# Kernel tuning notes

Hardware: AMD Instinct MI355X
Metric: run time of the kernel (lower is better)

## Reference

```python
import jax, jax.numpy as jnp
import numpy as np

V, E, HID, T = 50000, 512, 1024, 16   # vocab, embed_dim, hidden_dim, tagset
H = HID // 2                          # per-direction LSTM hidden
B, S = 32, 512                        # batch, seq_len
NEG = -10000.0                        # start/stop transitions are set to -10000 in __init__


def setup_inputs() -> dict:
    key = jax.random.key(0)
    ks = jax.random.split(key, 12)
    g = lambda i, shape, scale: (jax.random.normal(ks[i], shape, jnp.float32) * scale)
    return {
        "sentence": jax.random.randint(ks[0], (B, S), 0, V),
        "embedding": g(1, (V, E), 1.0),
        # PyTorch LSTM gate order i,f,g,o; bias fused (b_ih + b_hh)
        "Wih_f": g(2, (4 * H, E), 0.04), "Whh_f": g(3, (4 * H, H), 0.04), "b_f": g(4, (4 * H,), 0.04),
        "Wih_b": g(5, (4 * H, E), 0.04), "Whh_b": g(6, (4 * H, H), 0.04), "b_b": g(7, (4 * H,), 0.04),
        "W_out": g(8, (T, HID), 0.04), "b_out": g(9, (T,), 0.04),
        "transitions": g(10, (T, T), 0.35),   # xavier_normal-ish
        "start_trans": jnp.full((T,), NEG, jnp.float32),
        "stop_trans": jnp.full((T,), NEG, jnp.float32),
    }


def _lstm_dir(x, Wih, Whh, b, reverse):
    # x: [B, S, E] -> h sequence [B, S, H]
    bsz, hid = x.shape[0], Whh.shape[1]

    def step(carry, xt):
        h, c = carry
        gates = xt @ Wih.T + h @ Whh.T + b          # [B, 4H]
        i, f, gg, o = jnp.split(gates, 4, axis=-1)
        c = jax.nn.sigmoid(f) * c + jax.nn.sigmoid(i) * jnp.tanh(gg)
        h = jax.nn.sigmoid(o) * jnp.tanh(c)
        return (h, c), h

    init = (jnp.zeros((bsz, hid), x.dtype), jnp.zeros((bsz, hid), x.dtype))
    _, hs = jax.lax.scan(step, init, jnp.swapaxes(x, 0, 1), reverse=reverse)
    return jnp.swapaxes(hs, 0, 1)


def _features(sentence, embedding, Wih_f, Whh_f, b_f, Wih_b, Whh_b, b_b, W_out, b_out):
    emb = embedding[sentence]                                  # [B, S, E]
    hf = _lstm_dir(emb, Wih_f, Whh_f, b_f, reverse=False)      # [B, S, H]
    hb = _lstm_dir(emb, Wih_b, Whh_b, b_b, reverse=True)       # [B, S, H]
    return jnp.concatenate([hf, hb], -1) @ W_out.T + b_out     # [B, S, T]


def reference(sentence, embedding, Wih_f, Whh_f, b_f, Wih_b, Whh_b, b_b,
              W_out, b_out, transitions, start_trans, stop_trans):
    feats = _features(sentence, embedding, Wih_f, Whh_f, b_f,
                      Wih_b, Whh_b, b_b, W_out, b_out)         # [B, S, T]

    # ---- Viterbi DP (forward pass with backpointers) ----
    v0 = feats[:, 0] + start_trans                             # [B, T]

    def step(v, feat):
        scores = v[:, :, None] + transitions[None]             # [B, Tprev, Tcur]
        idx = jnp.argmax(scores, axis=1)                       # [B, T] backpointers
        v = jnp.max(scores, axis=1) + feat
        return v, idx

    v, idxs = jax.lax.scan(step, v0, jnp.swapaxes(feats[:, 1:], 0, 1))  # idxs: [S-1, B, T]
    last = jnp.argmax(v + stop_trans, axis=-1)                 # [B]

    # ---- backtrace ----
    def back(tag, idx):
        prev = jnp.take_along_axis(idx, tag[:, None], axis=1)[:, 0]
        return prev, prev

    _, prevs = jax.lax.scan(back, last, idxs, reverse=True)    # [S-1, B]
    tags = jnp.concatenate([jnp.swapaxes(prevs, 0, 1), last[:, None]], axis=1)  # [B, S]
    return tags
```

## Files before the change

kernel.cpp:

```cpp
#include <hip/hip_runtime.h>
#include <stdint.h>

#define BATCH 32
#define SEQ   512
#define EDIM  512
#define HID   512
#define NG    2048
#define NTAG  16

typedef _Float16 f16;
typedef _Float16 f16x4 __attribute__((ext_vector_type(4)));
typedef _Float16 f16x8 __attribute__((ext_vector_type(8)));
typedef float    f32x4 __attribute__((ext_vector_type(4)));

#define LO_SCALE 2048.0f
#define LO_INV   (1.0f/2048.0f)

__global__ __launch_bounds__(256) void k_split4(
    const float* __restrict__ s0, const float* __restrict__ s1,
    const float* __restrict__ s2, const float* __restrict__ s3,
    f16* __restrict__ wih_hi, f16* __restrict__ wih_lo,
    f16* __restrict__ whh_hi, f16* __restrict__ whh_lo) {
    const int y = blockIdx.y;
    const float* src = (y == 0) ? s0 : (y == 1) ? s1 : (y == 2) ? s2 : s3;
    f16* hi = ((y < 2) ? wih_hi : whh_hi) + (size_t)(y & 1) * NG * EDIM;
    f16* lo = ((y < 2) ? wih_lo : whh_lo) + (size_t)(y & 1) * NG * EDIM;
    int i = blockIdx.x * blockDim.x + threadIdx.x;
    int stride = gridDim.x * blockDim.x;
    for (; i < NG*EDIM; i += stride) {
        float x = src[i];
        f16 h = (f16)x;
        hi[i] = h;
        lo[i] = (f16)((x - (float)h) * LO_SCALE);
    }
}

__global__ __launch_bounds__(256) void k_gather(const int* __restrict__ sent,
                                                const float* __restrict__ emb,
                                                f16* __restrict__ ehi, f16* __restrict__ elo) {
    int m = blockIdx.x;
    int idx = sent[m];
    const float* src = emb + (size_t)idx * EDIM;
    int k = threadIdx.x * 2;
    float2 v = *(const float2*)(src + k);
    f16 h0 = (f16)v.x, h1 = (f16)v.y;
    ehi[(size_t)m*EDIM + k]     = h0;
    ehi[(size_t)m*EDIM + k + 1] = h1;
    elo[(size_t)m*EDIM + k]     = (f16)((v.x - (float)h0) * LO_SCALE);
    elo[(size_t)m*EDIM + k + 1] = (f16)((v.y - (float)h1) * LO_SCALE);
}

__device__ __forceinline__ void gld16(const void* g, void* l) {
    __builtin_amdgcn_global_load_lds((const __attribute__((address_space(1))) uint32_t*)g,
                                     (__attribute__((address_space(3))) uint32_t*)l, 16, 0, 0);
}
__device__ __forceinline__ f32x4 mfma16(f16x8 a, f16x8 b, f32x4 c) {
    return __builtin_amdgcn_mfma_f32_16x16x32_f16(a, b, c, 0, 0, 0);
}

__global__ __launch_bounds__(512, 1) void k_rec(
    const f16* __restrict__ ehi,  const f16* __restrict__ elo,
    const f16* __restrict__ Whhi, const f16* __restrict__ Whlo,
    const f16* __restrict__ Wihi, const f16* __restrict__ Wilo,
    const float* __restrict__ b_f, const float* __restrict__ b_b,
    unsigned* __restrict__ hx,
    float* __restrict__ h_hist)
{
    __shared__ char  hhiS[16384];
    __shared__ char  hloS[16384];
    __shared__ char  ehiS[16384];
    __shared__ char  eloS[16384];
    __shared__ float gbuf[2*4*16*17];

    const int wg    = blockIdx.x;
    const int dir   = wg >> 6;
    const int mt    = (wg >> 5) & 1;
    const int chunk = wg & 31;
    const int u0    = chunk * 16;
    const int tid   = threadIdx.x;
    const int lane  = tid & 63;
    const int wave  = tid >> 6;
    const int g     = wave & 3;
    const int kh    = wave >> 2;
    const int u     = lane & 15;
    const int q4    = lane >> 4;

    unsigned* hxd = hx + (size_t)dir * 2 * BATCH * HID;

    const int pbl = tid >> 4;
    const int pu  = tid & 15;
    const char* hrowH = hhiS + u*1024;
    const char* hrowL = hloS + u*1024;
    const char* erowH = ehiS + u*1024;
    const char* erowL = eloS + u*1024;
    const int u7 = u & 7;

    f16x8 bhv[8], blv[8], wbh[8], wbl[8];
    {
        const size_t row = (size_t)(dir*NG + g*512 + u0 + u) * EDIM;
        const f16* ph = Whhi + row + q4*8;
        const f16* pl = Whlo + row + q4*8;
        const f16* qh = Wihi + row + q4*8;
        const f16* ql = Wilo + row + q4*8;
        #pragma unroll
        for (int kt = 0; kt < 8; ++kt) {
            bhv[kt] = *(const f16x8*)(ph + (kh*8 + kt)*32);
            blv[kt] = *(const f16x8*)(pl + (kh*8 + kt)*32);
            wbh[kt] = *(const f16x8*)(qh + (kh*8 + kt)*32);
            wbl[kt] = *(const f16x8*)(ql + (kh*8 + kt)*32);
        }
    }

    float bv[4];
    {
        const float* bias = dir ? b_b : b_f;
        #pragma unroll
        for (int gg = 0; gg < 4; ++gg) bv[gg] = bias[gg*512 + u0 + pu];
    }

    const int grow0 = mt*16 + wave;
    const int srcu  = (lane ^ wave) * 8;

    float c = 0.0f;

    for (int t = 0; t < SEQ; ++t) {
        const int s = dir ? (SEQ - 1 - t) : t;

        {
            size_t r0 = ((size_t)(grow0)*SEQ + s) * EDIM + srcu;
            size_t r1 = ((size_t)(grow0 + 8)*SEQ + s) * EDIM + srcu;
            gld16(ehi + r0, ehiS + tid*16);
            gld16(ehi + r1, ehiS + 8192 + tid*16);
            gld16(elo + r0, eloS + tid*16);
            gld16(elo + r1, eloS + 8192 + tid*16);
        }

        if (t == 0) {
            #pragma unroll
            for (int i = 0; i < 4; ++i) {
                int q = i*512 + tid, row = q >> 7, kq = (q & 127)*4;
                int off = row*1024 + ((kq >> 3) ^ (row & 7))*16 + (kq & 4)*2;
                *(uint2*)(hhiS + off) = (uint2){0u, 0u};
                *(uint2*)(hloS + off) = (uint2){0u, 0u};
            }
        } else {
            const unsigned tag32 = ((unsigned)((t - 1) >> 1) & 3u) << 16;
            const unsigned* hsrc = hxd + (size_t)(t & 1)*BATCH*HID + (size_t)mt*16*HID;
            unsigned pend = 0xFu;
            while (pend) {
                unsigned long long va[4], vb[4];
                #pragma unroll
                for (int i = 0; i < 4; ++i) {
                    if (pend & (1u << i)) {
                        int q = i*512 + tid;
                        const unsigned long long* p =
                            (const unsigned long long*)(hsrc + (q >> 7)*HID + (q & 127)*4);
                        va[i] = __hip_atomic_load(p,     __ATOMIC_RELAXED, __HIP_MEMORY_SCOPE_AGENT);
                        vb[i] = __hip_atomic_load(p + 1, __ATOMIC_RELAXED, __HIP_MEMORY_SCOPE_AGENT);
                    }
                }
                #pragma unroll
                for (int i = 0; i < 4; ++i) {
                    if (!(pend & (1u << i))) continue;
                    unsigned w0 = (unsigned)va[i], w1 = (unsigned)(va[i] >> 32);
                    unsigned w2 = (unsigned)vb[i], w3 = (unsigned)(vb[i] >> 32);
                    if ((((w0 ^ tag32) | (w1 ^ tag32) | (w2 ^ tag32) | (w3 ^ tag32)) & 0x30000u) != 0u)
                        continue;
                    unsigned hi01 = (w0 & 0xffffu) | (w1 << 16);
                    unsigned hi23 = (w2 & 0xffffu) | (w3 << 16);
                    unsigned lo01 = (w0 >> 16) | (w1 & 0xffff0000u);
                    unsigned lo23 = (w2 >> 16) | (w3 & 0xffff0000u);
                    int q = i*512 + tid, row = q >> 7, kq = (q & 127)*4;
                    int off = row*1024 + ((kq >> 3) ^ (row & 7))*16 + (kq & 4)*2;
                    *(uint2*)(hhiS + off) = (uint2){hi01, hi23};
                    *(uint2*)(hloS + off) = (uint2){lo01, lo23};
                    pend &= ~(1u << i);
                }
            }
        }
        __syncthreads();

        f32x4 aH = {0.f,0.f,0.f,0.f}, aM1 = aH, aM2 = aH;
        #pragma unroll
        for (int kt = 0; kt < 8; ++kt) {
            int off = (((kh*8 + kt)*4 + q4) ^ u7) * 16;
            f16x8 eh = *(const f16x8*)(erowH + off);
            f16x8 el = *(const f16x8*)(erowL + off);
            f16x8 ah = *(const f16x8*)(hrowH + off);
            f16x8 al = *(const f16x8*)(hrowL + off);
            aH  = mfma16(eh, wbh[kt], aH);
            aM1 = mfma16(eh, wbl[kt], aM1);
            aM2 = mfma16(el, wbh[kt], aM2);
            aH  = mfma16(ah, bhv[kt], aH);
            aM1 = mfma16(ah, blv[kt], aM1);
            aM2 = mfma16(al, bhv[kt], aM2);
        }
        #pragma unroll
        for (int j = 0; j < 4; ++j) {
            int row = q4*4 + j;
            gbuf[(kh*4 + g)*272 + row*17 + u] = aH[j] + (aM1[j] + aM2[j]) * LO_INV;
        }
        __syncthreads();

        if (tid < 256) {
            float gs[4];
            #pragma unroll
            for (int gg = 0; gg < 4; ++gg)
                gs[gg] = gbuf[(0*4 + gg)*272 + pbl*17 + pu]
                       + gbuf[(1*4 + gg)*272 + pbl*17 + pu] + bv[gg];
            float si = 1.0f / (1.0f + __expf(-gs[0]));
            float sf = 1.0f / (1.0f + __expf(-gs[1]));
            float tg = 1.0f - 2.0f / (__expf(2.0f*gs[2]) + 1.0f);
            float so = 1.0f / (1.0f + __expf(-gs[3]));
            c = sf * c + si * tg;
            float hval = so * (1.0f - 2.0f / (__expf(2.0f*c) + 1.0f));
            f16 hh = (f16)hval;
            f16 hl = (f16)((hval - (float)hh) * LO_SCALE);
            unsigned packed = (unsigned)__builtin_bit_cast(unsigned short, hh)
                            | ((unsigned)__builtin_bit_cast(unsigned short, hl) << 16);
            packed = (packed & ~0x30000u) | ((((unsigned)t >> 1) & 3u) << 16);
            int b = mt*16 + pbl;
            unsigned* hdst = hxd + (size_t)((t + 1) & 1)*BATCH*HID + b*HID + u0 + pu;
            __hip_atomic_store(hdst, packed, __ATOMIC_RELAXED, __HIP_MEMORY_SCOPE_AGENT);
            __builtin_nontemporal_store(hval,
                h_hist + ((size_t)b*SEQ + s)*1024 + dir*HID + u0 + pu);
        }
    }
}

__global__ __launch_bounds__(256) void k_feats(
    const float* __restrict__ H,
    const float* __restrict__ Wout,
    const float* __restrict__ bout,
    float* __restrict__ feats)
{
    __shared__ float Wt[1024][16];
    int tid = threadIdx.x;
    for (int i = tid; i < 16384; i += 256)
        Wt[i & 1023][i >> 10] = Wout[i];
    __syncthreads();
    int wave = tid >> 6, lane = tid & 63;
    int row = blockIdx.x * 4 + wave;
    const float* hrow = H + (size_t)row * 1024;
    float acc[16];
    #pragma unroll
    for (int t = 0; t < 16; ++t) acc[t] = 0.f;
    #pragma unroll
    for (int cc = 0; cc < 4; ++cc) {
        float4 hv = *(const float4*)(hrow + cc*256 + lane*4);
        #pragma unroll
        for (int j = 0; j < 4; ++j) {
            int k = cc*256 + lane*4 + j;
            float h = (&hv.x)[j];
            #pragma unroll
            for (int tg = 0; tg < 16; ++tg) acc[tg] += h * Wt[k][tg];
        }
    }
    #pragma unroll
    for (int off = 32; off >= 1; off >>= 1) {
        #pragma unroll
        for (int tg = 0; tg < 16; ++tg) acc[tg] += __shfl_xor(acc[tg], off);
    }
    if (lane == 0) {
        #pragma unroll
        for (int tg = 0; tg < 16; ++tg)
            feats[(size_t)row*16 + tg] = acc[tg] + bout[tg];
    }
}

__global__ __launch_bounds__(64) void k_viterbi(
    const float* __restrict__ feats,
    const float* __restrict__ trans,
    const float* __restrict__ startt, const float* __restrict__ stopt,
    int* __restrict__ out)
{
    __shared__ float fs[SEQ*NTAG];
    __shared__ unsigned char bp[511*16];
    int b = blockIdx.x;
    int lane = threadIdx.x;
    {
        const float4* src = (const float4*)(feats + (size_t)b * SEQ * NTAG);
        float4* dst = (float4*)fs;
        for (int i = lane; i < SEQ*NTAG/4; i += 64) dst[i] = src[i];
    }
    int cur = lane & 15;
    int q   = lane >> 4;
    float tr[4];
    #pragma unroll
    for (int i = 0; i < 4; ++i) tr[i] = trans[(q*4 + i)*16 + cur];
    __syncthreads();
    float v = fs[cur] + startt[cur];
    for (int s = 1; s < SEQ; ++s) {
        float best = -1e30f; int bi = 0;
        #pragma unroll
        for (int i = 0; i < 4; ++i) {
            float pv = __shfl(v, q*4 + i);
            float sc = pv + tr[i];
            if (sc > best) { best = sc; bi = q*4 + i; }
        }
        #pragma unroll
        for (int off = 16; off <= 32; off <<= 1) {
            float ob = __shfl_xor(best, off);
            int   oi = __shfl_xor(bi, off);
            if (ob > best || (ob == best && oi < bi)) { best = ob; bi = oi; }
        }
        if (lane < 16) bp[(s - 1)*16 + cur] = (unsigned char)bi;
        v = best + fs[s*16 + cur];
    }
    float sc = v + stopt[cur];
    int bc = cur;
    #pragma unroll
    for (int off = 1; off <= 32; off <<= 1) {
        float os = __shfl_xor(sc, off);
        int   oc = __shfl_xor(bc, off);
        if (os > sc || (os == sc && oc < bc)) { sc = os; bc = oc; }
    }
    __syncthreads();
    if (lane == 0) {
        int curt = bc;
        out[b*SEQ + SEQ - 1] = curt;
        for (int s2 = SEQ - 2; s2 >= 0; --s2) {
            curt = bp[s2*16 + curt];
            out[b*SEQ + s2] = curt;
        }
    }
}

extern "C" void kernel_launch(void* const* d_in, const int* in_sizes, int n_in,
                              void* d_out, int out_size, void* d_ws, size_t ws_size,
                              hipStream_t stream) {
    (void)in_sizes; (void)n_in; (void)out_size; (void)ws_size;
    const int*   sentence  = (const int*)  d_in[0];
    const float* embedding = (const float*)d_in[1];
    const float* Wih_f = (const float*)d_in[2];
    const float* Whh_f = (const float*)d_in[3];
    const float* b_f   = (const float*)d_in[4];
    const float* Wih_b = (const float*)d_in[5];
    const float* Whh_b = (const float*)d_in[6];
    const float* b_b   = (const float*)d_in[7];
    const float* W_out = (const float*)d_in[8];
    const float* b_out = (const float*)d_in[9];
    const float* trans = (const float*)d_in[10];
    const float* startt= (const float*)d_in[11];
    const float* stopt = (const float*)d_in[12];

    char* ws = (char*)d_ws;
    float* h_hist = (float*)(ws);
    f16*   ehi    = (f16*)  (ws +  67108864ull);
    f16*   elo    = (f16*)  (ws +  83886080ull);
    f16*   wihhi  = (f16*)  (ws + 100663296ull);
    f16*   wihlo  = (f16*)  (ws + 104857600ull);
    f16*   whhhi  = (f16*)  (ws + 109051904ull);
    f16*   whhlo  = (f16*)  (ws + 113246208ull);
    unsigned* hx  = (unsigned*)(ws + 117440512ull);
    float* feats  = (float*)(ws + 117702656ull);

    hipMemsetAsync(hx, 0xFF, 262144, stream);

    k_split4<<<dim3(512, 4), 256, 0, stream>>>(Wih_f, Wih_b, Whh_f, Whh_b,
                                               wihhi, wihlo, whhhi, whhlo);
    k_gather<<<16384, 256, 0, stream>>>(sentence, embedding, ehi, elo);

    k_rec<<<128, 512, 0, stream>>>(ehi, elo, whhhi, whhlo, wihhi, wihlo,
                                   b_f, b_b, hx, h_hist);

    k_feats<<<4096, 256, 0, stream>>>(h_hist, W_out, b_out, feats);
    k_viterbi<<<32, 64, 0, stream>>>(feats, trans, startt, stopt, (int*)d_out);
}
```

Baseline: 2.227 ms.

## Split recurrent MFMA work over K across all eight waves, computing four gates each

Each wave used to own one gate and half of K. Now each wave owns one eighth of K and computes all four gates, so each LDS fragment of the embedding and hidden state is loaded once and reused across four gates. The partial sums go into a larger gate buffer laid out as float4 per gate, and the pointwise stage adds eight partials with vector loads. The aim is fewer LDS reads per MFMA and more independent accumulator chains. In exchange, the reduction has four times the partials and LDS use grows by 32KB.

```diff
diff --git a/kernel.cpp b/kernel.cpp
--- a/kernel.cpp
+++ b/kernel.cpp
@@ -70,7 +70,7 @@
     __shared__ char  hloS[16384];
     __shared__ char  ehiS[16384];
     __shared__ char  eloS[16384];
-    __shared__ float gbuf[2*4*16*17];
+    __shared__ float gbuf4[8*16*16*4];
 
     const int wg    = blockIdx.x;
     const int dir   = wg >> 6;
@@ -80,8 +80,7 @@
     const int tid   = threadIdx.x;
     const int lane  = tid & 63;
     const int wave  = tid >> 6;
-    const int g     = wave & 3;
-    const int kh    = wave >> 2;
+    const int kq    = wave;
     const int u     = lane & 15;
     const int q4    = lane >> 4;
 
@@ -95,19 +94,17 @@
     const char* erowL = eloS + u*1024;
     const int u7 = u & 7;
 
-    f16x8 bhv[8], blv[8], wbh[8], wbl[8];
-    {
+    f16x8 bhv[4][2], blv[4][2], wbh[4][2], wbl[4][2];
+    #pragma unroll
+    for (int g = 0; g < 4; ++g) {
         const size_t row = (size_t)(dir*NG + g*512 + u0 + u) * EDIM;
-        const f16* ph = Whhi + row + q4*8;
-        const f16* pl = Whlo + row + q4*8;
-        const f16* qh = Wihi + row + q4*8;
-        const f16* ql = Wilo + row + q4*8;
-        #pragma unroll
-        for (int kt = 0; kt < 8; ++kt) {
-            bhv[kt] = *(const f16x8*)(ph + (kh*8 + kt)*32);
-            blv[kt] = *(const f16x8*)(pl + (kh*8 + kt)*32);
-            wbh[kt] = *(const f16x8*)(qh + (kh*8 + kt)*32);
-            wbl[kt] = *(const f16x8*)(ql + (kh*8 + kt)*32);
+        #pragma unroll
+        for (int kt = 0; kt < 2; ++kt) {
+            const int off = (kq*2 + kt)*32 + q4*8;
+            bhv[g][kt] = *(const f16x8*)(Whhi + row + off);
+            blv[g][kt] = *(const f16x8*)(Whlo + row + off);
+            wbh[g][kt] = *(const f16x8*)(Wihi + row + off);
+            wbl[g][kt] = *(const f16x8*)(Wilo + row + off);
         }
     }
 
@@ -138,8 +135,8 @@
         if (t == 0) {
             #pragma unroll
             for (int i = 0; i < 4; ++i) {
-                int q = i*512 + tid, row = q >> 7, kq = (q & 127)*4;
-                int off = row*1024 + ((kq >> 3) ^ (row & 7))*16 + (kq & 4)*2;
+                int q = i*512 + tid, row = q >> 7, kqq = (q & 127)*4;
+                int off = row*1024 + ((kqq >> 3) ^ (row & 7))*16 + (kqq & 4)*2;
                 *(uint2*)(hhiS + off) = (uint2){0u, 0u};
                 *(uint2*)(hloS + off) = (uint2){0u, 0u};
             }
@@ -170,8 +167,8 @@
                     unsigned hi23 = (w2 & 0xffffu) | (w3 << 16);
                     unsigned lo01 = (w0 >> 16) | (w1 & 0xffff0000u);
                     unsigned lo23 = (w2 >> 16) | (w3 & 0xffff0000u);
-                    int q = i*512 + tid, row = q >> 7, kq = (q & 127)*4;
-                    int off = row*1024 + ((kq >> 3) ^ (row & 7))*16 + (kq & 4)*2;
+                    int q = i*512 + tid, row = q >> 7, kqq = (q & 127)*4;
+                    int off = row*1024 + ((kqq >> 3) ^ (row & 7))*16 + (kqq & 4)*2;
                     *(uint2*)(hhiS + off) = (uint2){hi01, hi23};
                     *(uint2*)(hloS + off) = (uint2){lo01, lo23};
                     pend &= ~(1u << i);
@@ -180,38 +177,48 @@
         }
         __syncthreads();
 
-        f32x4 aH = {0.f,0.f,0.f,0.f}, aM1 = aH, aM2 = aH;
-        #pragma unroll
-        for (int kt = 0; kt < 8; ++kt) {
-            int off = (((kh*8 + kt)*4 + q4) ^ u7) * 16;
+        f32x4 aH[4] = {}, aM1[4] = {}, aM2[4] = {};
+        #pragma unroll
+        for (int kt = 0; kt < 2; ++kt) {
+            int off = (((kq*2 + kt)*4 + q4) ^ u7) * 16;
             f16x8 eh = *(const f16x8*)(erowH + off);
             f16x8 el = *(const f16x8*)(erowL + off);
             f16x8 ah = *(const f16x8*)(hrowH + off);
             f16x8 al = *(const f16x8*)(hrowL + off);
-            aH  = mfma16(eh, wbh[kt], aH);
-            aM1 = mfma16(eh, wbl[kt], aM1);
-            aM2 = mfma16(el, wbh[kt], aM2);
-            aH  = mfma16(ah, bhv[kt], aH);
-            aM1 = mfma16(ah, blv[kt], aM1);
-            aM2 = mfma16(al, bhv[kt], aM2);
+            #pragma unroll
+            for (int g = 0; g < 4; ++g) {
+                aH[g]  = mfma16(eh, wbh[g][kt], aH[g]);
+                aM1[g] = mfma16(eh, wbl[g][kt], aM1[g]);
+                aM2[g] = mfma16(el, wbh[g][kt], aM2[g]);
+                aH[g]  = mfma16(ah, bhv[g][kt], aH[g]);
+                aM1[g] = mfma16(ah, blv[g][kt], aM1[g]);
+                aM2[g] = mfma16(al, bhv[g][kt], aM2[g]);
+            }
         }
         #pragma unroll
         for (int j = 0; j < 4; ++j) {
             int row = q4*4 + j;
-            gbuf[(kh*4 + g)*272 + row*17 + u] = aH[j] + (aM1[j] + aM2[j]) * LO_INV;
+            f32x4 v;
+            #pragma unroll
+            for (int g = 0; g < 4; ++g)
+                v[g] = aH[g][j] + (aM1[g][j] + aM2[g][j]) * LO_INV;
+            *(f32x4*)(gbuf4 + ((kq*16 + row)*16 + u)*4) = v;
         }
         __syncthreads();
 
         if (tid < 256) {
-            float gs[4];
-            #pragma unroll
-            for (int gg = 0; gg < 4; ++gg)
-                gs[gg] = gbuf[(0*4 + gg)*272 + pbl*17 + pu]
-                       + gbuf[(1*4 + gg)*272 + pbl*17 + pu] + bv[gg];
-            float si = 1.0f / (1.0f + __expf(-gs[0]));
-            float sf = 1.0f / (1.0f + __expf(-gs[1]));
-            float tg = 1.0f - 2.0f / (__expf(2.0f*gs[2]) + 1.0f);
-            float so = 1.0f / (1.0f + __expf(-gs[3]));
+            f32x4 sv = *(const f32x4*)(gbuf4 + ((0*16 + pbl)*16 + pu)*4);
+            #pragma unroll
+            for (int k2 = 1; k2 < 8; ++k2)
+                sv += *(const f32x4*)(gbuf4 + ((k2*16 + pbl)*16 + pu)*4);
+            float gi = sv[0] + bv[0];
+            float gf = sv[1] + bv[1];
+            float gg = sv[2] + bv[2];
+            float go = sv[3] + bv[3];
+            float si = 1.0f / (1.0f + __expf(-gi));
+            float sf = 1.0f / (1.0f + __expf(-gf));
+            float tg = 1.0f - 2.0f / (__expf(2.0f*gg) + 1.0f);
+            float so = 1.0f / (1.0f + __expf(-go));
             c = sf * c + si * tg;
             float hval = so * (1.0f - 2.0f / (__expf(2.0f*c) + 1.0f));
             f16 hh = (f16)hval;
```

Measured after the change: 2.497 ms. +12.1%, slower.

## Split LSTM batch across four workgroup groups and amortize output-projection weight loads

Applied to the files above, without the earlier changes.

The recurrent kernel now runs 256 workgroups instead of 128, each handling 8 batch rows instead of 16. This halves the per-step embedding and hidden-state traffic and the gate nonlinearity work per workgroup, shortening the latency-bound serial step. The cost is that half of each 16-row MFMA tile is now redundant, and twice as many workgroups take part in the cross-workgroup spin-wait handoff. The feature-projection kernel now processes 64 rows per block instead of 4, so the W_out transpose into shared memory happens far fewer times.

```diff
diff --git a/kernel.cpp b/kernel.cpp
--- a/kernel.cpp
+++ b/kernel.cpp
@@ -66,17 +66,18 @@
     unsigned* __restrict__ hx,
     float* __restrict__ h_hist)
 {
-    __shared__ char  hhiS[16384];
-    __shared__ char  hloS[16384];
-    __shared__ char  ehiS[16384];
-    __shared__ char  eloS[16384];
+    __shared__ char  hhiS[8192];
+    __shared__ char  hloS[8192];
+    __shared__ char  ehiS[8192];
+    __shared__ char  eloS[8192];
     __shared__ float gbuf[2*4*16*17];
 
     const int wg    = blockIdx.x;
-    const int dir   = wg >> 6;
-    const int mt    = (wg >> 5) & 1;
+    const int dir   = wg >> 7;
+    const int mq    = (wg >> 5) & 3;
     const int chunk = wg & 31;
     const int u0    = chunk * 16;
+    const int b0    = mq * 8;
     const int tid   = threadIdx.x;
     const int lane  = tid & 63;
     const int wave  = tid >> 6;
@@ -89,10 +90,10 @@
 
     const int pbl = tid >> 4;
     const int pu  = tid & 15;
-    const char* hrowH = hhiS + u*1024;
-    const char* hrowL = hloS + u*1024;
-    const char* erowH = ehiS + u*1024;
-    const char* erowL = eloS + u*1024;
+    const char* hrowH = hhiS + (u & 7)*1024;
+    const char* hrowL = hloS + (u & 7)*1024;
+    const char* erowH = ehiS + (u & 7)*1024;
+    const char* erowL = eloS + (u & 7)*1024;
     const int u7 = u & 7;
 
     f16x8 bhv[8], blv[8], wbh[8], wbl[8];
@@ -118,8 +119,8 @@
         for (int gg = 0; gg < 4; ++gg) bv[gg] = bias[gg*512 + u0 + pu];
     }
 
-    const int grow0 = mt*16 + wave;
-    const int srcu  = (lane ^ wave) * 8;
+    const int grow = b0 + wave;
+    const int srcu = (lane ^ wave) * 8;
 
     float c = 0.0f;
 
@@ -127,30 +128,27 @@
         const int s = dir ? (SEQ - 1 - t) : t;
 
         {
-            size_t r0 = ((size_t)(grow0)*SEQ + s) * EDIM + srcu;
-            size_t r1 = ((size_t)(grow0 + 8)*SEQ + s) * EDIM + srcu;
+            size_t r0 = ((size_t)grow*SEQ + s) * EDIM + srcu;
             gld16(ehi + r0, ehiS + tid*16);
-            gld16(ehi + r1, ehiS + 8192 + tid*16);
             gld16(elo + r0, eloS + tid*16);
-            gld16(elo + r1, eloS + 8192 + tid*16);
         }
 
         if (t == 0) {
             #pragma unroll
-            for (int i = 0; i < 4; ++i) {
-                int q = i*512 + tid, row = q >> 7, kq = (q & 127)*4;
-                int off = row*1024 + ((kq >> 3) ^ (row & 7))*16 + (kq & 4)*2;
+            for (int i = 0; i < 2; ++i) {
+                int q = i*512 + tid, row = q >> 7, kqq = (q & 127)*4;
+                int off = row*1024 + ((kqq >> 3) ^ row)*16 + (kqq & 4)*2;
                 *(uint2*)(hhiS + off) = (uint2){0u, 0u};
                 *(uint2*)(hloS + off) = (uint2){0u, 0u};
             }
         } else {
             const unsigned tag32 = ((unsigned)((t - 1) >> 1) & 3u) << 16;
-            const unsigned* hsrc = hxd + (size_t)(t & 1)*BATCH*HID + (size_t)mt*16*HID;
-            unsigned pend = 0xFu;
+            const unsigned* hsrc = hxd + (size_t)(t & 1)*BATCH*HID + (size_t)b0*HID;
+            unsigned pend = 0x3u;
             while (pend) {
-                unsigned long long va[4], vb[4];
+                unsigned long long va[2], vb[2];
                 #pragma unroll
-                for (int i = 0; i < 4; ++i) {
+                for (int i = 0; i < 2; ++i) {
                     if (pend & (1u << i)) {
                         int q = i*512 + tid;
                         const unsigned long long* p =
@@ -160,7 +158,7 @@
                     }
                 }
                 #pragma unroll
-                for (int i = 0; i < 4; ++i) {
+                for (int i = 0; i < 2; ++i) {
                     if (!(pend & (1u << i))) continue;
                     unsigned w0 = (unsigned)va[i], w1 = (unsigned)(va[i] >> 32);
                     unsigned w2 = (unsigned)vb[i], w3 = (unsigned)(vb[i] >> 32);
@@ -170,8 +168,8 @@
                     unsigned hi23 = (w2 & 0xffffu) | (w3 << 16);
                     unsigned lo01 = (w0 >> 16) | (w1 & 0xffff0000u);
                     unsigned lo23 = (w2 >> 16) | (w3 & 0xffff0000u);
-                    int q = i*512 + tid, row = q >> 7, kq = (q & 127)*4;
-                    int off = row*1024 + ((kq >> 3) ^ (row & 7))*16 + (kq & 4)*2;
+                    int q = i*512 + tid, row = q >> 7, kqq = (q & 127)*4;
+                    int off = row*1024 + ((kqq >> 3) ^ row)*16 + (kqq & 4)*2;
                     *(uint2*)(hhiS + off) = (uint2){hi01, hi23};
                     *(uint2*)(hloS + off) = (uint2){lo01, lo23};
                     pend &= ~(1u << i);
@@ -202,7 +200,7 @@
         }
         __syncthreads();
 
-        if (tid < 256) {
+        if (tid < 128) {
             float gs[4];
             #pragma unroll
             for (int gg = 0; gg < 4; ++gg)
@@ -219,7 +217,7 @@
             unsigned packed = (unsigned)__builtin_bit_cast(unsigned short, hh)
                             | ((unsigned)__builtin_bit_cast(unsigned short, hl) << 16);
             packed = (packed & ~0x30000u) | ((((unsigned)t >> 1) & 3u) << 16);
-            int b = mt*16 + pbl;
+            int b = b0 + pbl;
             unsigned* hdst = hxd + (size_t)((t + 1) & 1)*BATCH*HID + b*HID + u0 + pu;
             __hip_atomic_store(hdst, packed, __ATOMIC_RELAXED, __HIP_MEMORY_SCOPE_AGENT);
             __builtin_nontemporal_store(hval,
@@ -240,31 +238,36 @@
         Wt[i & 1023][i >> 10] = Wout[i];
     __syncthreads();
     int wave = tid >> 6, lane = tid & 63;
-    int row = blockIdx.x * 4 + wave;
-    const float* hrow = H + (size_t)row * 1024;
-    float acc[16];
+    float bo[16];
     #pragma unroll
-    for (int t = 0; t < 16; ++t) acc[t] = 0.f;
-    #pragma unroll
-    for (int cc = 0; cc < 4; ++cc) {
-        float4 hv = *(const float4*)(hrow + cc*256 + lane*4);
-        #pragma unroll
-        for (int j = 0; j < 4; ++j) {
-            int k = cc*256 + lane*4 + j;
-            float h = (&hv.x)[j];
-            #pragma unroll
-            for (int tg = 0; tg < 16; ++tg) acc[tg] += h * Wt[k][tg];
-        }
-    }
-    #pragma unroll
-    for (int off = 32; off >= 1; off >>= 1) {
-        #pragma unroll
-        for (int tg = 0; tg < 16; ++tg) acc[tg] += __shfl_xor(acc[tg], off);
-    }
-    if (lane == 0) {
-        #pragma unroll
-        for (int tg = 0; tg < 16; ++tg)
-            feats[(size_t)row*16 + tg] = acc[tg] + bout[tg];
+    for (int tg = 0; tg < 16; ++tg) bo[tg] = bout[tg];
+    for (int r = 0; r < 16; ++r) {
+        int row = blockIdx.x * 64 + wave * 16 + r;
+        const float* hrow = H + (size_t)row * 1024;
+        float acc[16];
+        #pragma unroll
+        for (int t = 0; t < 16; ++t) acc[t] = 0.f;
+        #pragma unroll
+        for (int cc = 0; cc < 4; ++cc) {
+            float4 hv = *(const float4*)(hrow + cc*256 + lane*4);
+            #pragma unroll
+            for (int j = 0; j < 4; ++j) {
+                int k = cc*256 + lane*4 + j;
+                float h = (&hv.x)[j];
+                #pragma unroll
+                for (int tg = 0; tg < 16; ++tg) acc[tg] += h * Wt[k][tg];
+            }
+        }
+        #pragma unroll
+        for (int off = 32; off >= 1; off >>= 1) {
+            #pragma unroll
+            for (int tg = 0; tg < 16; ++tg) acc[tg] += __shfl_xor(acc[tg], off);
+        }
+        if (lane == 0) {
+            #pragma unroll
+            for (int tg = 0; tg < 16; ++tg)
+                feats[(size_t)row*16 + tg] = acc[tg] + bo[tg];
+        }
     }
 }
 
@@ -361,9 +364,9 @@
                                                wihhi, wihlo, whhhi, whhlo);
     k_gather<<<16384, 256, 0, stream>>>(sentence, embedding, ehi, elo);
 
-    k_rec<<<128, 512, 0, stream>>>(ehi, elo, whhhi, whhlo, wihhi, wihlo,
+    k_rec<<<256, 512, 0, stream>>>(ehi, elo, whhhi, whhlo, wihhi, wihlo,
                                    b_f, b_b, hx, h_hist);
 
-    k_feats<<<4096, 256, 0, stream>>>(h_hist, W_out, b_out, feats);
+    k_feats<<<256, 256, 0, stream>>>(h_hist, W_out, b_out, feats);
     k_viterbi<<<32, 64, 0, stream>>>(feats, trans, startt, stopt, (int*)d_out);
 }
```

After: 2.075 ms. -6.8%, faster.
